# Optimization experiments

Hardware: AMD Instinct MI355X
Metric: run time of the kernel (lower is better)

Reference implementation:

```python
import jax, jax.numpy as jnp
import numpy as np

GAMMAK = 1.0 / 256.0  # 1/(2*d) so kernel values don't underflow for unit-gaussian data


def setup_inputs() -> dict:
    key = jax.random.key(0)
    k1, k2, k3, k4, k5 = jax.random.split(key, 5)
    N, d = 8192, 128
    X = jax.random.normal(k1, (N, d), dtype=jnp.float32)
    y = jax.random.normal(k2, (N - 1, d), dtype=jnp.float32)
    y_next = jax.random.normal(k3, (N - 1, d), dtype=jnp.float32)
    # reset_transform initializes R=eye, t=0; perturb slightly for nontrivial math
    R = jnp.eye(d, dtype=jnp.float32) + 0.01 * jax.random.normal(k4, (d, d), dtype=jnp.float32)
    t = 0.01 * jax.random.normal(k5, (d, 1), dtype=jnp.float32)
    return {"X": X, "y": y, "y_next": y_next, "R": R, "t": t}


def reference(X, y, y_next, R, t):
    # _transform_pts: (R @ y.T + t).T == y @ R.T + t.squeeze()
    yt = y @ R.T + t[:, 0]            # (N-1, d)
    Xb = X[:-1]                        # (N-1, d) kernel base points
    # pairwise_sqeuclidean(Xb, yt), clamped at 0
    sq = jnp.clip(
        jnp.sum(Xb * Xb, axis=1)[:, None]
        + jnp.sum(yt * yt, axis=1)[None, :]
        - 2.0 * (Xb @ yt.T),
        0.0, None,
    )                                  # (N-1, N-1)
    G = jnp.exp(-GAMMAK * sq)
    # diag(1/rowsum) @ G  ==  G / rowsum[:, None]  (avoids explicit NxN diagonal)
    y_pred = (G / jnp.sum(G, axis=1, keepdims=True)) @ X[1:]  # (N-1, d)
    return y_pred
```

## Files before the change

### kernel.cpp

```cpp
#include <hip/hip_runtime.h>
#include <hip/hip_bf16.h>


#define LOG2E 1.44269504088896340736f
#define KNEG (-(1.0f/256.0f)*LOG2E)
#define KA2C (2.0f*(1.0f/256.0f)*LOG2E)

typedef __attribute__((ext_vector_type(4)))  float f32x4;
typedef __attribute__((ext_vector_type(16))) float f32x16;
typedef __attribute__((ext_vector_type(8)))  short bf16x8;

__device__ __forceinline__ unsigned short f2bf(float f) {
  unsigned u = __builtin_bit_cast(unsigned, f);
  u = (u + 0x7fffu + ((u >> 16) & 1u)) >> 16;
  return (unsigned short)u;
}
__device__ __forceinline__ unsigned pk2bf(float a, float b) {
  __hip_bfloat162 h = __float22bfloat162_rn(float2{a, b});
  unsigned u;
  __builtin_memcpy(&u, &h, 4);
  return u;
}
__device__ __forceinline__ bf16x8 pack8(float4 p0, float4 p1) {
  uint4 u;
  u.x = pk2bf(p0.x, p0.y); u.y = pk2bf(p0.z, p0.w);
  u.z = pk2bf(p1.x, p1.y); u.w = pk2bf(p1.z, p1.w);
  return __builtin_bit_cast(bf16x8, u);
}
__device__ __forceinline__ float fast_exp2(float x) {
#if __has_builtin(__builtin_amdgcn_exp2f)
  return __builtin_amdgcn_exp2f(x);
#else
  return exp2f(x);
#endif
}
__device__ __forceinline__ void gl2lds16(const void* g, void* l) {
  __builtin_amdgcn_global_load_lds((const __attribute__((address_space(1))) unsigned int*)g,
                                   (__attribute__((address_space(3))) unsigned int*)l, 16, 0, 0);
}
__device__ __forceinline__ f32x16 mfma_32x32x16(bf16x8 a, bf16x8 b, f32x16 c) {
  return __builtin_amdgcn_mfma_f32_32x32x16_bf16(a, b, c, 0, 0, 0);
}
__device__ __forceinline__ void pl32swap(unsigned &a, unsigned &b) {
#if __has_builtin(__builtin_amdgcn_permlane32_swap)
  auto r = __builtin_amdgcn_permlane32_swap((int)a, (int)b, false, false);
  a = (unsigned)r[0];
  b = (unsigned)r[1];
#else
  unsigned pa = (unsigned)__shfl_xor((int)a, 32, 64);
  unsigned pb = (unsigned)__shfl_xor((int)b, 32, 64);
  bool hi = (threadIdx.x & 32) != 0;
  unsigned na = hi ? pb : a;
  unsigned nb = hi ? b  : pa;
  a = na; b = nb;
#endif
}

#define T_STRIDE 34816
#define V_OFF    18432

__global__ __launch_bounds__(64) void k_prep(const float* __restrict__ y,
                                             const float* __restrict__ R,
                                             const float* __restrict__ t,
                                             const float* __restrict__ X,
                                             unsigned short* __restrict__ ctp) {
  __shared__ char slice[8704];
  const int task = blockIdx.x;
  const int ln = threadIdx.x;
  const int l = ln & 31, h = ln >> 5;

  if (task < 256) {
    unsigned short* ytt = (unsigned short*)slice;
    float* ynf = (float*)(slice + 8448);
    const int T = task >> 1, jcw = task & 1;
    const int rw = task * 32;
    bf16x8 af[8];
    {
      int row = rw + l; if (row > 8190) row = 8190;
      const float* yr = y + (size_t)row * 128;
#pragma unroll
      for (int kc = 0; kc < 8; ++kc) {
        float4 p0 = *(const float4*)(yr + kc*16 + 8*h);
        float4 p1 = *(const float4*)(yr + kc*16 + 8*h + 4);
        af[kc] = pack8(p0, p1);
      }
    }
    f32x16 ac[4];
#pragma unroll
    for (int cc=0; cc<4; ++cc)
#pragma unroll
      for (int i=0;i<16;++i) ac[cc][i] = 0.f;
#pragma unroll
    for (int cc=0; cc<4; ++cc) {
      const float* Rr = R + (size_t)(cc*32 + l) * 128;
#pragma unroll
      for (int kc=0; kc<8; ++kc) {
        float4 p0 = *(const float4*)(Rr + kc*16 + 8*h);
        float4 p1 = *(const float4*)(Rr + kc*16 + 8*h + 4);
        ac[cc] = mfma_32x32x16(af[kc], pack8(p0, p1), ac[cc]);
      }
    }
    float tv0 = t[l], tv1 = t[32+l], tv2 = t[64+l], tv3 = t[96+l];
    float v0[16], v1[16], v2[16], v3[16], ssq[16];
#pragma unroll
    for (int r=0;r<16;++r) {
      v0[r]=ac[0][r]+tv0; v1[r]=ac[1][r]+tv1; v2[r]=ac[2][r]+tv2; v3[r]=ac[3][r]+tv3;
      ssq[r] = v0[r]*v0[r] + v1[r]*v1[r] + v2[r]*v2[r] + v3[r]*v3[r];
    }
#pragma unroll
    for (int off=1; off<32; off<<=1)
#pragma unroll
      for (int r=0;r<16;++r) ssq[r] += __shfl_xor(ssq[r], off, 64);
    if (l < 16) {
      int r = l;
      int grow = rw + (r&3) + 8*(r>>2) + 4*h;
      ynf[(r&3) + 8*(r>>2) + 4*h] = (grow >= 8191) ? -1.0e4f : KNEG * ssq[r];
    }
#pragma unroll
    for (int r=0;r<16;++r) {
      int rloc = (r&3) + 8*(r>>2) + 4*h;
      ytt[rloc*132 +   0 + l] = f2bf(KA2C * v0[r]);
      ytt[rloc*132 +  32 + l] = f2bf(KA2C * v1[r]);
      ytt[rloc*132 +  64 + l] = f2bf(KA2C * v2[r]);
      ytt[rloc*132 +  96 + l] = f2bf(KA2C * v3[r]);
    }
    __syncthreads();
    char* base = (char*)ctp + (size_t)T*T_STRIDE;
#pragma unroll
    for (int kc=0;kc<8;++kc) {
      const unsigned short* s = &ytt[l*132 + kc*16 + 8*h];
      uint2 a = *(const uint2*)(s);
      uint2 b = *(const uint2*)(s + 4);
      uint4 o; o.x=a.x; o.y=a.y; o.z=b.x; o.w=b.y;
      *(uint4*)(base + (jcw*9 + kc)*1024 + ln*16) = o;
    }
    {
      float yn = ynf[l];
      unsigned short hi = f2bf(yn);
      float hif = __builtin_bit_cast(float, (unsigned)hi << 16);
      unsigned short lo = f2bf(yn - hif);
      uint4 o; o.x = (h == 0) ? ((unsigned)hi | ((unsigned)lo << 16)) : 0u;
      o.y = 0u; o.z = 0u; o.w = 0u;
      *(uint4*)(base + (jcw*9 + 8)*1024 + ln*16) = o;
    }
  } else {
    unsigned short* xs = (unsigned short*)slice;
    const int tv_ = task - 256;
    const int T2 = tv_ >> 1, half = tv_ & 1;
    const int xr0 = T2*64 + half*32 + 1;
    {
      int rl = ln >> 1, ch2 = ln & 1;
      int row = xr0 + rl; if (row > 8191) row = 8191;
      const float* src = X + (size_t)row*128 + ch2*64;
      unsigned short* dst = xs + rl*136 + ch2*64;
#pragma unroll
      for (int i=0;i<8;++i) {
        float4 p0 = *(const float4*)(src + i*8);
        float4 p1 = *(const float4*)(src + i*8 + 4);
        uint4 w;
        w.x = pk2bf(p0.x, p0.y); w.y = pk2bf(p0.z, p0.w);
        w.z = pk2bf(p1.x, p1.y); w.w = pk2bf(p1.z, p1.w);
        *(uint4*)(dst + i*8) = w;
      }
    }
    __syncthreads();
    char* base = (char*)ctp + (size_t)T2*T_STRIDE + V_OFF;
#pragma unroll
    for (int ch=0; ch<8; ++ch) {
      int jcl = ch >> 2, cc = ch & 3;
      int lr0 = jcl*16 + 8*h;
      int c = cc*32 + l;
      uint4 o;
      o.x = (unsigned)xs[(lr0+0)*136 + c] | ((unsigned)xs[(lr0+1)*136 + c] << 16);
      o.y = (unsigned)xs[(lr0+2)*136 + c] | ((unsigned)xs[(lr0+3)*136 + c] << 16);
      o.z = (unsigned)xs[(lr0+4)*136 + c] | ((unsigned)xs[(lr0+5)*136 + c] << 16);
      o.w = (unsigned)xs[(lr0+6)*136 + c] | ((unsigned)xs[(lr0+7)*136 + c] << 16);
      int jc16 = half*2 + jcl;
      *(uint4*)(base + (jc16*4 + cc)*1024 + ln*16) = o;
    }
  }
}

__global__ __launch_bounds__(256, 2) void k_main(
    const float* __restrict__ X,
    const unsigned short* __restrict__ ctp,
    float* __restrict__ accp,
    float* __restrict__ rsp,
    int js) {
  __shared__ unsigned short stg[2][T_STRIDE/2];
  const int tid = threadIdx.x;
  const int wv = tid >> 6, ln = tid & 63;
  const int l = ln & 31, h = ln >> 5;
  const int row = blockIdx.x*128 + wv*32 + l;

  bf16x8 qf[9];
  {
    const float* xr = X + (size_t)row * 128;
#pragma unroll
    for (int kc=0;kc<8;++kc) {
      float4 p0 = *(const float4*)(xr + kc*16 + 8*h);
      float4 p1 = *(const float4*)(xr + kc*16 + 8*h + 4);
      qf[kc] = pack8(p0, p1);
    }
    uint4 o; o.x = (h == 0) ? 0x3F803F80u : 0u; o.y = 0u; o.z = 0u; o.w = 0u;
    qf[8] = __builtin_bit_cast(bf16x8, o);
  }
  f32x16 acc[4];
#pragma unroll
  for (int cc=0;cc<4;++cc)
#pragma unroll
    for (int i=0;i<16;++i) acc[cc][i]=0.f;
  float rs = 0.f;
  const int sp = blockIdx.y;
  const int Tbeg = (sp * 128) / js;
  const int Tend = ((sp + 1) * 128) / js;

  auto dosm = [&](const f32x16& sa, unsigned wx[4], unsigned wy[4]) {
#pragma unroll
    for (int rg=0; rg<4; ++rg) {
      float g0 = fast_exp2(sa[rg*4+0]);
      float g1 = fast_exp2(sa[rg*4+1]);
      float g2 = fast_exp2(sa[rg*4+2]);
      float g3 = fast_exp2(sa[rg*4+3]);
      rs += (g0+g1) + (g2+g3);
      wx[rg] = pk2bf(g0, g1);
      wy[rg] = pk2bf(g2, g3);
    }
  };
  auto dopv = [&](const char* sb, int jcb, unsigned wx[4], unsigned wy[4]) {
#pragma unroll
    for (int jj=0; jj<2; ++jj) {
      unsigned ax = wx[2*jj], bx = wx[2*jj+1];
      unsigned ay = wy[2*jj], by = wy[2*jj+1];
      pl32swap(ax, bx);
      pl32swap(ay, by);
      uint4 gv; gv.x = ax; gv.y = ay; gv.z = bx; gv.w = by;
      bf16x8 pb = __builtin_bit_cast(bf16x8, gv);
#pragma unroll
      for (int cc=0;cc<4;++cc) {
        bf16x8 a2 = *(const bf16x8*)(sb + V_OFF + ((jcb+jj)*4+cc)*1024 + ln*16);
        acc[cc] = mfma_32x32x16(a2, pb, acc[cc]);
      }
    }
  };

  {
    const char* cb = (const char*)ctp + (size_t)Tbeg*T_STRIDE;
#pragma unroll
    for (int i=0;i<9;++i) {
      int c = wv + 4*i;
      if (c < 34) gl2lds16(cb + c*1024 + ln*16, (char*)stg + c*1024);
    }
  }
  __syncthreads();

  int cur = 0;
  for (int T = Tbeg; T < Tend; ++T) {
    const char* sb = (const char*)stg + cur*T_STRIDE;
    if (T+1 < Tend) {
      const char* nb = (const char*)ctp + (size_t)(T+1)*T_STRIDE;
      char* sn = (char*)stg + (cur^1)*T_STRIDE;
#pragma unroll
      for (int i=0;i<9;++i) {
        int c = wv + 4*i;
        if (c < 34) gl2lds16(nb + c*1024 + ln*16, sn + c*1024);
      }
    }

    f32x16 sa0, sa1;
#pragma unroll
    for (int i=0;i<16;++i) { sa0[i]=0.f; sa1[i]=0.f; }
#pragma unroll
    for (int kc=0;kc<9;++kc) {
      bf16x8 a0 = *(const bf16x8*)(sb + kc*1024 + ln*16);
      sa0 = mfma_32x32x16(a0, qf[kc], sa0);
    }
#pragma unroll
    for (int kc=0;kc<9;++kc) {
      bf16x8 a1 = *(const bf16x8*)(sb + (9+kc)*1024 + ln*16);
      sa1 = mfma_32x32x16(a1, qf[kc], sa1);
    }
    unsigned wx0[4], wy0[4], wx1[4], wy1[4];
    dosm(sa0, wx0, wy0);
    dosm(sa1, wx1, wy1);
    dopv(sb, 0, wx0, wy0);
    dopv(sb, 2, wx1, wy1);

    __syncthreads();
    cur ^= 1;
  }
  rs += __shfl_xor(rs, 32, 64);
  if (h == 0) rsp[(size_t)sp*8192 + row] = rs;
#pragma unroll
  for (int cc=0;cc<4;++cc)
#pragma unroll
    for (int r=0;r<16;++r) {
      int c = cc*32 + (r&3) + 8*(r>>2) + 4*h;
      accp[((size_t)sp*128 + c)*8192 + row] = acc[cc][r];
    }
}

__global__ __launch_bounds__(256) void k_fin(const float* __restrict__ accp,
                                             const float* __restrict__ rsp,
                                             float* __restrict__ out,
                                             int js) {
  __shared__ float tr[64*36];
  __shared__ float rinv[64];
  const int tid = threadIdx.x;
  const int r0 = blockIdx.x * 64;
  const int c0 = blockIdx.y * 32;
  if (tid < 64) {
    float s = 0.f;
    for (int sp=0; sp<js; ++sp) s += rsp[(size_t)sp*8192 + r0 + tid];
    rinv[tid] = 1.f / s;
  }
  const int rq = tid & 15, cg = tid >> 4;
  float v[2][4];
#pragma unroll
  for (int cc=0;cc<2;++cc)
#pragma unroll
    for (int k=0;k<4;++k) v[cc][k]=0.f;
#pragma unroll 4
  for (int sp=0; sp<js; ++sp) {
    const float* base = accp + ((size_t)sp*128 + c0 + cg*2)*8192 + r0 + rq*4;
    float4 p0 = *(const float4*)(base);
    float4 p1 = *(const float4*)(base + 8192);
    v[0][0]+=p0.x; v[0][1]+=p0.y; v[0][2]+=p0.z; v[0][3]+=p0.w;
    v[1][0]+=p1.x; v[1][1]+=p1.y; v[1][2]+=p1.z; v[1][3]+=p1.w;
  }
  __syncthreads();
#pragma unroll
  for (int cc=0;cc<2;++cc)
#pragma unroll
    for (int k=0;k<4;++k)
      tr[(rq*4+k)*36 + cg*2+cc] = v[cc][k] * rinv[rq*4+k];
  __syncthreads();
  {
    int r = tid >> 2, q = tid & 3;
    int grow = r0 + r;
    if (grow < 8191) {
      float* dst = out + (size_t)grow*128 + c0 + q*8;
      const float* s2 = &tr[r*36 + q*8];
      *(float4*)(dst)     = *(const float4*)(s2);
      *(float4*)(dst + 4) = *(const float4*)(s2 + 4);
    }
  }
}

extern "C" void kernel_launch(void* const* d_in, const int* in_sizes, int n_in,
                              void* d_out, int out_size, void* d_ws, size_t ws_size,
                              hipStream_t stream) {
  const float* X = (const float*)d_in[0];
  const float* y = (const float*)d_in[1];
  const float* R = (const float*)d_in[3];
  const float* t = (const float*)d_in[4];
  float* out = (float*)d_out;
  char* ws = (char*)d_ws;

  unsigned short* ctp = (unsigned short*)ws;
  size_t rspoff = (size_t)128 * T_STRIDE;
  float* rsp  = (float*)(ws + rspoff);
  size_t accoff = rspoff + 512*1024;
  float* accp = (float*)(ws + accoff);

  int js = 8;
  while (js > 1 && accoff + (size_t)js*128*8192*4 > ws_size) js >>= 1;

  k_prep<<<dim3(512), dim3(64), 0, stream>>>(y, R, t, X, ctp);
  k_main<<<dim3(64, js), dim3(256), 0, stream>>>(X, ctp, accp, rsp, js);
  k_fin<<<dim3(128, 4), dim3(256), 0, stream>>>(accp, rsp, out, js);
}
```

Measured before the change: 130.6 us.

## Stream V tiles from global into registers, shrink LDS staging, raise occupancy

The V (X[1:]) operand of the PV matmul is now loaded straight from global memory into registers in two halves, and only the transformed-y score tile goes through the LDS double buffer. This roughly halves the LDS footprint per block so launch bounds can ask for three blocks per CU. The S and PV stages are interleaved per 32-column half, and the split-K factor js goes from 8 to 12. The risk is global-load latency on V that is no longer prefetched, more register pressure, and a larger partial-sum buffer and reduction in k_fin. With js=12, the while loop that halves js may reduce it to 6 instead of 4 when workspace is short, and Tbeg/Tend split 128 tiles unevenly across the 12 splits.

Result: slower. 139.9 us (+7.1%).

```diff
diff --git a/kernel.cpp b/kernel.cpp
--- a/kernel.cpp
+++ b/kernel.cpp
@@ -58,6 +58,7 @@
 
 #define T_STRIDE 34816
 #define V_OFF    18432
+#define YT_BYTES 18432
 
 __global__ __launch_bounds__(64) void k_prep(const float* __restrict__ y,
                                              const float* __restrict__ R,
@@ -181,13 +182,13 @@
   }
 }
 
-__global__ __launch_bounds__(256, 2) void k_main(
+__global__ __launch_bounds__(256, 3) void k_main(
     const float* __restrict__ X,
     const unsigned short* __restrict__ ctp,
     float* __restrict__ accp,
     float* __restrict__ rsp,
     int js) {
-  __shared__ unsigned short stg[2][T_STRIDE/2];
+  __shared__ unsigned short stg[2][YT_BYTES/2];
   const int tid = threadIdx.x;
   const int wv = tid >> 6, ln = tid & 63;
   const int l = ln & 31, h = ln >> 5;
@@ -227,7 +228,18 @@
       wy[rg] = pk2bf(g2, g3);
     }
   };
-  auto dopv = [&](const char* sb, int jcb, unsigned wx[4], unsigned wy[4]) {
+  auto doS = [&](const char* sb, int jc) -> f32x16 {
+    f32x16 sa;
+#pragma unroll
+    for (int i=0;i<16;++i) sa[i]=0.f;
+#pragma unroll
+    for (int kc=0;kc<9;++kc) {
+      bf16x8 a = *(const bf16x8*)(sb + (jc*9+kc)*1024 + ln*16);
+      sa = mfma_32x32x16(a, qf[kc], sa);
+    }
+    return sa;
+  };
+  auto dopv = [&](const bf16x8* v, unsigned wx[4], unsigned wy[4]) {
 #pragma unroll
     for (int jj=0; jj<2; ++jj) {
       unsigned ax = wx[2*jj], bx = wx[2*jj+1];
@@ -237,54 +249,52 @@
       uint4 gv; gv.x = ax; gv.y = ay; gv.z = bx; gv.w = by;
       bf16x8 pb = __builtin_bit_cast(bf16x8, gv);
 #pragma unroll
-      for (int cc=0;cc<4;++cc) {
-        bf16x8 a2 = *(const bf16x8*)(sb + V_OFF + ((jcb+jj)*4+cc)*1024 + ln*16);
-        acc[cc] = mfma_32x32x16(a2, pb, acc[cc]);
-      }
+      for (int cc=0;cc<4;++cc)
+        acc[cc] = mfma_32x32x16(v[jj*4+cc], pb, acc[cc]);
     }
   };
 
   {
     const char* cb = (const char*)ctp + (size_t)Tbeg*T_STRIDE;
 #pragma unroll
-    for (int i=0;i<9;++i) {
+    for (int i=0;i<5;++i) {
       int c = wv + 4*i;
-      if (c < 34) gl2lds16(cb + c*1024 + ln*16, (char*)stg + c*1024);
+      if (c < 18) gl2lds16(cb + c*1024 + ln*16, (char*)stg + c*1024);
     }
   }
   __syncthreads();
 
   int cur = 0;
   for (int T = Tbeg; T < Tend; ++T) {
-    const char* sb = (const char*)stg + cur*T_STRIDE;
+    const char* sb = (const char*)stg + cur*YT_BYTES;
+    const char* vb = (const char*)ctp + (size_t)T*T_STRIDE + V_OFF;
+
+    bf16x8 vlo[8];
+#pragma unroll
+    for (int c=0;c<8;++c) vlo[c] = *(const bf16x8*)(vb + c*1024 + ln*16);
+
     if (T+1 < Tend) {
       const char* nb = (const char*)ctp + (size_t)(T+1)*T_STRIDE;
-      char* sn = (char*)stg + (cur^1)*T_STRIDE;
-#pragma unroll
-      for (int i=0;i<9;++i) {
+      char* sn = (char*)stg + (cur^1)*YT_BYTES;
+#pragma unroll
+      for (int i=0;i<5;++i) {
         int c = wv + 4*i;
-        if (c < 34) gl2lds16(nb + c*1024 + ln*16, sn + c*1024);
+        if (c < 18) gl2lds16(nb + c*1024 + ln*16, sn + c*1024);
       }
     }
 
-    f32x16 sa0, sa1;
-#pragma unroll
-    for (int i=0;i<16;++i) { sa0[i]=0.f; sa1[i]=0.f; }
-#pragma unroll
-    for (int kc=0;kc<9;++kc) {
-      bf16x8 a0 = *(const bf16x8*)(sb + kc*1024 + ln*16);
-      sa0 = mfma_32x32x16(a0, qf[kc], sa0);
-    }
-#pragma unroll
-    for (int kc=0;kc<9;++kc) {
-      bf16x8 a1 = *(const bf16x8*)(sb + (9+kc)*1024 + ln*16);
-      sa1 = mfma_32x32x16(a1, qf[kc], sa1);
-    }
     unsigned wx0[4], wy0[4], wx1[4], wy1[4];
+    f32x16 sa0 = doS(sb, 0);
     dosm(sa0, wx0, wy0);
+    dopv(vlo, wx0, wy0);
+
+    bf16x8 vhi[8];
+#pragma unroll
+    for (int c=0;c<8;++c) vhi[c] = *(const bf16x8*)(vb + (8+c)*1024 + ln*16);
+
+    f32x16 sa1 = doS(sb, 1);
     dosm(sa1, wx1, wy1);
-    dopv(sb, 0, wx0, wy0);
-    dopv(sb, 2, wx1, wy1);
+    dopv(vhi, wx1, wy1);
 
     __syncthreads();
     cur ^= 1;
@@ -363,7 +373,7 @@
   size_t accoff = rspoff + 512*1024;
   float* accp = (float*)(ws + accoff);
 
-  int js = 8;
+  int js = 12;
   while (js > 1 && accoff + (size_t)js*128*8192*4 > ws_size) js >>= 1;
 
   k_prep<<<dim3(512), dim3(64), 0, stream>>>(y, R, t, X, ctp);
```
